# Performance work log

Measured on AMD Instinct MI355X. Metric: run time of the kernel, lower is better.

Reference implementation:

```python
import jax, jax.numpy as jnp
import numpy as np

NUM_HEADS = 8
WIN = 7  # local_window_size
HALF = WIN // 2


def setup_inputs() -> dict:
    key = jax.random.key(0)
    k1, k2, k3 = jax.random.split(key, 3)
    B, N, C = 1, 4096, 384  # N = T*H*W with T=4, H=W=32
    x = jax.random.normal(k1, (B, N, C), dtype=jnp.float32)
    w_qkv = jax.random.normal(k2, (C, 3 * C), dtype=jnp.float32) * 0.02
    w_proj = jax.random.normal(k3, (C, C), dtype=jnp.float32) * 0.02
    b_proj = jnp.zeros((C,), dtype=jnp.float32)
    return {"x": x, "w_qkv": w_qkv, "w_proj": w_proj, "b_proj": b_proj, "H": 32, "W": 32}


def _gather_windows(t):
    H, W = t.shape[3], t.shape[4]
    tp = jnp.pad(t, ((0, 0), (0, 0), (0, 0), (HALF, HALF), (HALF, HALF), (0, 0)))
    wins = [tp[:, :, :, dy:dy + H, dx:dx + W, :] for dy in range(WIN) for dx in range(WIN)]
    return jnp.stack(wins, axis=5)


def reference(x, w_qkv, w_proj, b_proj, H, W):
    B, N, C = x.shape
    nh, hd = NUM_HEADS, C // NUM_HEADS
    T = N // (H * W)
    scale = hd ** (-0.5)

    qkv = (x @ w_qkv).reshape(B, N, 3, nh, hd)
    # (B, nh, T, H, W, hd)
    q = qkv[:, :, 0].transpose(0, 2, 1, 3).reshape(B, nh, T, H, W, hd)
    k = qkv[:, :, 1].transpose(0, 2, 1, 3).reshape(B, nh, T, H, W, hd)
    v = qkv[:, :, 2].transpose(0, 2, 1, 3).reshape(B, nh, T, H, W, hd)

    kwin = _gather_windows(k)  # (B, nh, T, H, W, 49, hd); zeros at borders (NOT masked)
    vwin = _gather_windows(v)

    scores = jnp.einsum('bnthwd,bnthwkd->bnthwk', q, kwin) * scale
    attn = jax.nn.softmax(scores, axis=-1)  # zero-padded keys give score 0 -> weight exp(0)
    out = jnp.einsum('bnthwk,bnthwkd->bnthwd', attn, vwin)

    out = out.transpose(0, 2, 3, 4, 1, 5).reshape(B, N, C)
    return out @ w_proj + b_proj
```

## Files before the change

### kernel.cpp

```cpp
#include <hip/hip_runtime.h>
#include <hip/hip_bf16.h>
#include <math.h>

#define NH 8
#define HD 48
#define C_DIM 384
#define C3 1152
#define SCALE_F 0.14433756729740643f

typedef unsigned short ushort_t;
typedef __attribute__((ext_vector_type(8))) short short8;
typedef __attribute__((ext_vector_type(4))) float f32x4;

static __device__ __forceinline__ ushort_t bf16u(float f) {
    __hip_bfloat16 b = __float2bfloat16(f);
    return *(ushort_t*)&b;
}

__global__ __launch_bounds__(256) void split_bf16_kernel(const float* __restrict__ in,
                                                         ushort_t* __restrict__ hi,
                                                         ushort_t* __restrict__ lo,
                                                         int n4)
{
    const int i = blockIdx.x * 256 + threadIdx.x;
    if (i >= n4) return;
    const float4 v = ((const float4*)in)[i];
    const float f[4] = {v.x, v.y, v.z, v.w};
    ushort_t hb[4], lb[4];
    #pragma unroll
    for (int j = 0; j < 4; ++j) {
        __hip_bfloat16 h = __float2bfloat16(f[j]);
        __hip_bfloat16 l = __float2bfloat16(f[j] - __bfloat162float(h));
        hb[j] = *(ushort_t*)&h;
        lb[j] = *(ushort_t*)&l;
    }
    *(ushort4*)(hi + i * 4) = make_ushort4(hb[0], hb[1], hb[2], hb[3]);
    *(ushort4*)(lo + i * 4) = make_ushort4(lb[0], lb[1], lb[2], lb[3]);
}

__global__ __launch_bounds__(256) void split_wT_kernel(const float* __restrict__ w,
                                                       ushort_t* __restrict__ hiT,
                                                       ushort_t* __restrict__ loT,
                                                       int K, int N)
{
    const int idx = blockIdx.x * 256 + threadIdx.x;
    if (idx >= K * N) return;
    const int k = idx / N;
    const int n = idx - k * N;
    const float v = w[idx];
    __hip_bfloat16 h = __float2bfloat16(v);
    __hip_bfloat16 l = __float2bfloat16(v - __bfloat162float(h));
    hiT[n * K + k] = *(ushort_t*)&h;
    loT[n * K + k] = *(ushort_t*)&l;
}

__global__ __launch_bounds__(256) void gemm_mfma3(const ushort_t* __restrict__ Ah,
                                                  const ushort_t* __restrict__ Al,
                                                  const ushort_t* __restrict__ BhT,
                                                  const ushort_t* __restrict__ BlT,
                                                  const float* __restrict__ bias,
                                                  float* __restrict__ C,
                                                  int N, int K)
{
    __shared__ ushort_t sAh[128 * 40];
    __shared__ ushort_t sAl[128 * 40];
    __shared__ ushort_t sBh[64 * 40];
    __shared__ ushort_t sBl[64 * 40];

    const int tid = threadIdx.x;
    const int bm = blockIdx.x * 128;
    const int bn = blockIdx.y * 64;

    const int rowA = tid >> 2;
    const int slotA = (tid & 3) * 8;
    const int rowB = tid >> 2;
    const int slotB = (tid & 3) * 8;

    const ushort_t* gAh0 = Ah + (size_t)(bm + rowA) * K + slotA;
    const ushort_t* gAh1 = Ah + (size_t)(bm + rowA + 64) * K + slotA;
    const ushort_t* gAl0 = Al + (size_t)(bm + rowA) * K + slotA;
    const ushort_t* gAl1 = Al + (size_t)(bm + rowA + 64) * K + slotA;
    const ushort_t* gBh  = BhT + (size_t)(bn + rowB) * K + slotB;
    const ushort_t* gBl  = BlT + (size_t)(bn + rowB) * K + slotB;

    const int lane = tid & 63;
    const int wid = tid >> 6;
    const int wm = wid >> 1;
    const int wn = wid & 1;
    const int fr = lane & 15;
    const int kb = lane >> 4;
    const int aoff = (wm * 64 + fr) * 40 + kb * 8;
    const int boff = (wn * 32 + fr) * 40 + kb * 8;

    f32x4 acc[4][2] = {};

    for (int k0 = 0; k0 < K; k0 += 32) {
        const short8 va0 = *(const short8*)(gAh0 + k0);
        const short8 va1 = *(const short8*)(gAh1 + k0);
        const short8 vl0 = *(const short8*)(gAl0 + k0);
        const short8 vl1 = *(const short8*)(gAl1 + k0);
        const short8 vb0 = *(const short8*)(gBh + k0);
        const short8 vb1 = *(const short8*)(gBl + k0);
        *(short8*)&sAh[rowA * 40 + slotA]        = va0;
        *(short8*)&sAh[(rowA + 64) * 40 + slotA] = va1;
        *(short8*)&sAl[rowA * 40 + slotA]        = vl0;
        *(short8*)&sAl[(rowA + 64) * 40 + slotA] = vl1;
        *(short8*)&sBh[rowB * 40 + slotB]        = vb0;
        *(short8*)&sBl[rowB * 40 + slotB]        = vb1;
        __syncthreads();

        short8 ah[4], al[4], bh[2], bl[2];
        #pragma unroll
        for (int m = 0; m < 4; ++m) {
            ah[m] = *(const short8*)&sAh[aoff + m * 16 * 40];
            al[m] = *(const short8*)&sAl[aoff + m * 16 * 40];
        }
        #pragma unroll
        for (int n = 0; n < 2; ++n) {
            bh[n] = *(const short8*)&sBh[boff + n * 16 * 40];
            bl[n] = *(const short8*)&sBl[boff + n * 16 * 40];
        }
        #pragma unroll
        for (int m = 0; m < 4; ++m) {
            #pragma unroll
            for (int n = 0; n < 2; ++n) {
                acc[m][n] = __builtin_amdgcn_mfma_f32_16x16x32_bf16(ah[m], bh[n], acc[m][n], 0, 0, 0);
                acc[m][n] = __builtin_amdgcn_mfma_f32_16x16x32_bf16(ah[m], bl[n], acc[m][n], 0, 0, 0);
                acc[m][n] = __builtin_amdgcn_mfma_f32_16x16x32_bf16(al[m], bh[n], acc[m][n], 0, 0, 0);
            }
        }
        __syncthreads();
    }

    #pragma unroll
    for (int n = 0; n < 2; ++n) {
        const int col = bn + wn * 32 + n * 16 + fr;
        const float bv = bias ? bias[col] : 0.f;
        #pragma unroll
        for (int m = 0; m < 4; ++m) {
            const int r0 = bm + wm * 64 + m * 16 + kb * 4;
            #pragma unroll
            for (int r = 0; r < 4; ++r) {
                C[(size_t)(r0 + r) * N + col] = acc[m][n][r] + bv;
            }
        }
    }
}

__global__ __launch_bounds__(256) void gemm64(const float* __restrict__ A,
                                              const float* __restrict__ B,
                                              const float* __restrict__ bias,
                                              float* __restrict__ C,
                                              int M, int N, int K)
{
    __shared__ float As[64][17];
    __shared__ float Bs[16][64];

    const int tid = threadIdx.x;
    const int tx = tid & 15;
    const int ty = tid >> 4;
    const int bm = blockIdx.x * 64;
    const int bn = blockIdx.y * 64;
    const int arow = tid >> 2;
    const int acol = (tid & 3) << 2;
    const int brow = tid >> 4;
    const int bcol = (tid & 15) << 2;

    float acc[4][4] = {};

    for (int k0 = 0; k0 < K; k0 += 16) {
        const float4 a4 = *(const float4*)(A + (size_t)(bm + arow) * K + k0 + acol);
        const float4 b4 = *(const float4*)(B + (size_t)(k0 + brow) * N + bn + bcol);
        As[arow][acol + 0] = a4.x; As[arow][acol + 1] = a4.y;
        As[arow][acol + 2] = a4.z; As[arow][acol + 3] = a4.w;
        *(float4*)&Bs[brow][bcol] = b4;
        __syncthreads();
        #pragma unroll
        for (int kk = 0; kk < 16; ++kk) {
            const float a0 = As[ty * 4 + 0][kk];
            const float a1 = As[ty * 4 + 1][kk];
            const float a2 = As[ty * 4 + 2][kk];
            const float a3 = As[ty * 4 + 3][kk];
            const float4 b = *(const float4*)&Bs[kk][tx * 4];
            acc[0][0] = fmaf(a0, b.x, acc[0][0]); acc[0][1] = fmaf(a0, b.y, acc[0][1]);
            acc[0][2] = fmaf(a0, b.z, acc[0][2]); acc[0][3] = fmaf(a0, b.w, acc[0][3]);
            acc[1][0] = fmaf(a1, b.x, acc[1][0]); acc[1][1] = fmaf(a1, b.y, acc[1][1]);
            acc[1][2] = fmaf(a1, b.z, acc[1][2]); acc[1][3] = fmaf(a1, b.w, acc[1][3]);
            acc[2][0] = fmaf(a2, b.x, acc[2][0]); acc[2][1] = fmaf(a2, b.y, acc[2][1]);
            acc[2][2] = fmaf(a2, b.z, acc[2][2]); acc[2][3] = fmaf(a2, b.w, acc[2][3]);
            acc[3][0] = fmaf(a3, b.x, acc[3][0]); acc[3][1] = fmaf(a3, b.y, acc[3][1]);
            acc[3][2] = fmaf(a3, b.z, acc[3][2]); acc[3][3] = fmaf(a3, b.w, acc[3][3]);
        }
        __syncthreads();
    }

    float4 bb = {0.f, 0.f, 0.f, 0.f};
    if (bias) bb = *(const float4*)(bias + bn + tx * 4);
    #pragma unroll
    for (int i = 0; i < 4; ++i) {
        float4 o;
        o.x = acc[i][0] + bb.x; o.y = acc[i][1] + bb.y;
        o.z = acc[i][2] + bb.z; o.w = acc[i][3] + bb.w;
        *(float4*)(C + (size_t)(bm + ty * 4 + i) * N + bn + tx * 4) = o;
    }
}

#define KP_SHORTS 18432
#define PROW 72
__global__ __launch_bounds__(512) void local_attn_mfma5(const float* __restrict__ qkv,
                                                        ushort_t* __restrict__ outHi,
                                                        ushort_t* __restrict__ outLo)
{
    __shared__ ushort_t sKP[KP_SHORTS];
    __shared__ ushort_t sV[13504];
    __shared__ ushort_t sQ[2048];
    __shared__ float    sS[32 * 57];

    const int tid = threadIdx.x;
    const int b = blockIdx.x;
    const int t = b >> 8, h = (b >> 3) & 31, head = b & 7;

    if (tid < 288) {
        if (tid < 256) ((unsigned int*)(sKP + 17920))[tid] = 0u;
        else           ((unsigned int*)(sV + 13440))[tid - 256] = 0u;
    }

    #pragma unroll
    for (int it = 0; it < 2; ++it) {
        const int i = tid + it * 512;
        const int q = i >> 5, d = (i & 31) * 2;
        float2 v = make_float2(0.f, 0.f);
        if (d < 48)
            v = *(const float2*)(qkv + (size_t)((t << 10) + (h << 5) + q) * C3 + head * HD + d);
        const unsigned int pk = (unsigned int)bf16u(v.x * SCALE_F) | ((unsigned int)bf16u(v.y * SCALE_F) << 16);
        *(unsigned int*)&sQ[q * 64 + (d ^ ((q & 7) << 3))] = pk;
    }
    #pragma unroll
    for (int r = 0; r < 7; ++r) {
        const int hk = h + r - 3;
        const bool rowok = (unsigned)hk < 32u;
        const size_t rk = (size_t)((t << 10) + (hk << 5)) * C3 + C_DIM + head * HD;
        for (int i = tid; i < 1280; i += 512) {
            const int slot = i >> 5, d = (i & 31) * 2;
            const int c = slot - 3;
            float2 v = make_float2(0.f, 0.f);
            if (rowok && (unsigned)c < 32u && d < 48)
                v = *(const float2*)(qkv + rk + (size_t)c * C3 + d);
            const unsigned int pk = (unsigned int)bf16u(v.x) | ((unsigned int)bf16u(v.y) << 16);
            *(unsigned int*)&sKP[(r * 40 + slot) * 64 + (d ^ ((slot & 7) << 3))] = pk;
        }
    }
    __syncthreads();

    const int wv = tid >> 6, l = tid & 63, lr = l & 15, lc = l >> 4;

    float2 vreg[7][2];
    #pragma unroll
    for (int r = 0; r < 7; ++r) {
        const int hk = h + r - 3;
        const bool rowok = (unsigned)hk < 32u;
        const size_t rv = (size_t)((t << 10) + (hk << 5)) * C3 + 2 * C_DIM + head * HD;
        #pragma unroll
        for (int it = 0; it < 2; ++it) {
            const int i = tid + it * 512;
            float2 v = make_float2(0.f, 0.f);
            if (i < 960) {
                const int slot = i / 24;
                const int d = (i - slot * 24) * 2;
                const int c = slot - 3;
                if (rowok && (unsigned)c < 32u)
                    v = *(const float2*)(qkv + rv + (size_t)c * C3 + d);
            }
            vreg[r][it] = v;
        }
    }
    {
        short8 aq[2][2];
        #pragma unroll
        for (int fm = 0; fm < 2; ++fm) {
            const int q = fm * 16 + lr;
            aq[fm][0] = *(const short8*)&sQ[q * 64 + ((lc * 8) ^ ((q & 7) << 3))];
            aq[fm][1] = *(const short8*)&sQ[q * 64 + ((lc * 8 + 32) ^ ((q & 7) << 3))];
        }
        for (int u = wv; u < 21; u += 8) {
            const int r = u / 3, fn = u - r * 3;
            const int slot = fn * 16 + lr;
            const short8 b0 = *(const short8*)&sKP[(r * 40 + slot) * 64 + ((lc * 8) ^ ((slot & 7) << 3))];
            const short8 b1 = *(const short8*)&sKP[(r * 40 + slot) * 64 + ((lc * 8 + 32) ^ ((slot & 7) << 3))];
            f32x4 acc0 = {}, acc1 = {};
            acc0 = __builtin_amdgcn_mfma_f32_16x16x32_bf16(aq[0][0], b0, acc0, 0, 0, 0);
            acc0 = __builtin_amdgcn_mfma_f32_16x16x32_bf16(aq[0][1], b1, acc0, 0, 0, 0);
            acc1 = __builtin_amdgcn_mfma_f32_16x16x32_bf16(aq[1][0], b0, acc1, 0, 0, 0);
            acc1 = __builtin_amdgcn_mfma_f32_16x16x32_bf16(aq[1][1], b1, acc1, 0, 0, 0);
            #pragma unroll
            for (int reg = 0; reg < 4; ++reg) {
                const int q0 = lc * 4 + reg;
                const int dx0 = slot - q0;
                if (dx0 >= 0 && dx0 < 7) sS[q0 * 57 + r * 7 + dx0] = acc0[reg];
                const int q1 = 16 + lc * 4 + reg;
                const int dx1 = slot - q1;
                if (dx1 >= 0 && dx1 < 7) sS[q1 * 57 + r * 7 + dx1] = acc1[reg];
            }
        }
    }
    __syncthreads();

    #pragma unroll
    for (int r = 0; r < 7; ++r) {
        #pragma unroll
        for (int it = 0; it < 2; ++it) {
            const int i = tid + it * 512;
            if (i < 960) {
                const int slot = i / 24;
                const int d = (i - slot * 24) * 2;
                sV[(r * 48 + d) * 40 + slot]     = bf16u(vreg[r][it].x);
                sV[(r * 48 + d + 1) * 40 + slot] = bf16u(vreg[r][it].y);
            }
        }
    }
    if (tid < 32) {
        const int q = tid;
        float sv[49];
        #pragma unroll
        for (int j = 0; j < 49; ++j) sv[j] = sS[q * 57 + j];
        float mx = sv[0];
        #pragma unroll
        for (int j = 1; j < 49; ++j) mx = fmaxf(mx, sv[j]);
        float sum = 0.f;
        #pragma unroll
        for (int j = 0; j < 49; ++j) { sv[j] = __expf(sv[j] - mx); sum += sv[j]; }
        const float inv = 1.f / sum;
        #pragma unroll
        for (int j = 0; j < 49; ++j) {
            const int r = j / 7, dx = j - (j / 7) * 7;
            sKP[(r * 32 + q) * PROW + q + dx] = bf16u(sv[j] * inv);
        }
    } else {
        for (int i = tid - 32; i < 7 * 32 * PROW; i += 480) {
            const int row = i / PROW;
            const int col = i - row * PROW;
            const int q = row & 31;
            if ((unsigned)(col - q) >= 7u)
                sKP[i] = 0;
        }
    }
    __syncthreads();

    if (wv < 6) {
        const int fm = (wv >= 3) ? 1 : 0;
        const int fn = wv - fm * 3;
        const int q = fm * 16 + lr;
        const int dim = fn * 16 + lr;
        f32x4 acc = {};
        #pragma unroll
        for (int r = 0; r < 7; ++r) {
            const short8 a0 = *(const short8*)&sKP[(r * 32 + q) * PROW + lc * 8];
            const short8 a1 = *(const short8*)&sKP[(r * 32 + q) * PROW + lc * 8 + 32];
            const short8 b0 = *(const short8*)&sV[(r * 48 + dim) * 40 + lc * 8];
            const short8 b1 = *(const short8*)&sV[(r * 48 + dim) * 40 + lc * 8 + 32];
            acc = __builtin_amdgcn_mfma_f32_16x16x32_bf16(a0, b0, acc, 0, 0, 0);
            acc = __builtin_amdgcn_mfma_f32_16x16x32_bf16(a1, b1, acc, 0, 0, 0);
        }
        #pragma unroll
        for (int reg = 0; reg < 4; ++reg) {
            const int qq = fm * 16 + lc * 4 + reg;
            const int n = (t << 10) | (h << 5) | qq;
            const float o = acc[reg];
            __hip_bfloat16 hb = __float2bfloat16(o);
            __hip_bfloat16 lb = __float2bfloat16(o - __bfloat162float(hb));
            const size_t ob = (size_t)n * C_DIM + head * HD + dim;
            outHi[ob] = *(ushort_t*)&hb;
            outLo[ob] = *(ushort_t*)&lb;
        }
    }
}

__global__ __launch_bounds__(256) void local_attn16(const float* __restrict__ qkv,
                                                    float* __restrict__ out)
{
    const int tid = threadIdx.x;
    const int dlane = tid & 15;
    const int gid = blockIdx.x * 16 + (tid >> 4);
    const int head = gid & 7;
    const int n = gid >> 3;
    const int t = n >> 10;
    const int h = (n >> 5) & 31;
    const int w = n & 31;
    const float scale = SCALE_F;

    const float* qp = qkv + (size_t)n * C3 + head * HD;
    const float q0 = qp[dlane];
    const float q1 = qp[dlane + 16];
    const float q2 = qp[dlane + 32];

    const size_t base_k = (size_t)(C_DIM + head * HD);
    const size_t base_v = (size_t)(2 * C_DIM + head * HD);

    float s[49];
    #pragma unroll
    for (int p = 0; p < 49; ++p) {
        const int dy = p / 7, dx = p % 7;
        const int hk = h + dy - 3;
        const int wk = w + dx - 3;
        float sc = 0.f;
        if ((unsigned)hk < 32u && (unsigned)wk < 32u) {
            const int nk = (t << 10) | (hk << 5) | wk;
            const float* kp = qkv + (size_t)nk * C3 + base_k;
            float acc = q0 * kp[dlane];
            acc = fmaf(q1, kp[dlane + 16], acc);
            acc = fmaf(q2, kp[dlane + 32], acc);
            acc += __shfl_xor(acc, 1, 16);
            acc += __shfl_xor(acc, 2, 16);
            acc += __shfl_xor(acc, 4, 16);
            acc += __shfl_xor(acc, 8, 16);
            sc = acc * scale;
        }
        s[p] = sc;
    }

    float m = s[0];
    #pragma unroll
    for (int p = 1; p < 49; ++p) m = fmaxf(m, s[p]);
    float sum = 0.f;
    #pragma unroll
    for (int p = 0; p < 49; ++p) { s[p] = __expf(s[p] - m); sum += s[p]; }
    const float inv = 1.f / sum;

    float o0 = 0.f, o1 = 0.f, o2 = 0.f;
    #pragma unroll
    for (int p = 0; p < 49; ++p) {
        const int dy = p / 7, dx = p % 7;
        const int hk = h + dy - 3;
        const int wk = w + dx - 3;
        if ((unsigned)hk < 32u && (unsigned)wk < 32u) {
            const float wgt = s[p] * inv;
            const int nk = (t << 10) | (hk << 5) | wk;
            const float* vp = qkv + (size_t)nk * C3 + base_v;
            o0 = fmaf(wgt, vp[dlane],      o0);
            o1 = fmaf(wgt, vp[dlane + 16], o1);
            o2 = fmaf(wgt, vp[dlane + 32], o2);
        }
    }

    float* op = out + (size_t)n * C_DIM + head * HD;
    op[dlane]      = o0;
    op[dlane + 16] = o1;
    op[dlane + 32] = o2;
}

extern "C" void kernel_launch(void* const* d_in, const int* in_sizes, int n_in,
                              void* d_out, int out_size, void* d_ws, size_t ws_size,
                              hipStream_t stream)
{
    const float* x      = (const float*)d_in[0];
    const float* w_qkv  = (const float*)d_in[1];
    const float* w_proj = (const float*)d_in[2];
    const float* b_proj = (const float*)d_in[3];

    const int M = 4096;
    dim3 blk(256);

    const size_t NEED = 33226752;

    unsigned char* ws = (unsigned char*)d_ws;
    float* qkv = (float*)ws;
    float* att = (float*)(ws + 18874368);

    if (ws_size >= NEED) {
        ushort_t* Ah  = (ushort_t*)(ws + 25165824);
        ushort_t* Al  = (ushort_t*)(ws + 28311552);
        ushort_t* BhT = (ushort_t*)(ws + 31457280);
        ushort_t* BlT = (ushort_t*)(ws + 32342016);

        split_bf16_kernel<<<dim3(1536), blk, 0, stream>>>(x, Ah, Al, M * C_DIM / 4);
        split_wT_kernel<<<dim3((C_DIM * C3 + 255) / 256), blk, 0, stream>>>(w_qkv, BhT, BlT, C_DIM, C3);
        gemm_mfma3<<<dim3(M / 128, C3 / 64), blk, 0, stream>>>(Ah, Al, BhT, BlT, nullptr, qkv, C3, C_DIM);

        local_attn_mfma5<<<dim3(1024), dim3(512), 0, stream>>>(qkv, Ah, Al);

        split_wT_kernel<<<dim3((C_DIM * C_DIM + 255) / 256), blk, 0, stream>>>(w_proj, BhT, BlT, C_DIM, C_DIM);
        gemm_mfma3<<<dim3(M / 128, C_DIM / 64), blk, 0, stream>>>(Ah, Al, BhT, BlT, b_proj, (float*)d_out, C_DIM, C_DIM);
    } else {
        gemm64<<<dim3(M / 64, C3 / 64), blk, 0, stream>>>(x, w_qkv, nullptr, qkv, M, C3, C_DIM);
        local_attn16<<<dim3(2048), blk, 0, stream>>>(qkv, att);
        gemm64<<<dim3(M / 64, C_DIM / 64), blk, 0, stream>>>(att, w_proj, b_proj, (float*)d_out, M, C_DIM, C_DIM);
    }
}
```

Baseline: 91.83 us.

## Merge split kernels into one launch and remap GEMM blocks across XCDs

Combines the three fp32-to-bf16 hi/lo split kernels (x, w_qkv, w_proj) into a single launch, giving w_proj its own workspace buffers so it no longer has to be split after attention. Both GEMMs switch to a 1D grid with a workgroup remap that spreads consecutive block IDs across the 8 XCDs before decoding tile coordinates. The aim is fewer kernel launches and better L2 locality per XCD. It needs slightly more workspace, and the remap assumes the grid size is divisible by 8.

```diff
diff --git a/kernel.cpp b/kernel.cpp
--- a/kernel.cpp
+++ b/kernel.cpp
@@ -17,25 +17,50 @@
     return *(ushort_t*)&b;
 }
 
-__global__ __launch_bounds__(256) void split_bf16_kernel(const float* __restrict__ in,
-                                                         ushort_t* __restrict__ hi,
-                                                         ushort_t* __restrict__ lo,
-                                                         int n4)
-{
-    const int i = blockIdx.x * 256 + threadIdx.x;
-    if (i >= n4) return;
-    const float4 v = ((const float4*)in)[i];
-    const float f[4] = {v.x, v.y, v.z, v.w};
-    ushort_t hb[4], lb[4];
-    #pragma unroll
-    for (int j = 0; j < 4; ++j) {
-        __hip_bfloat16 h = __float2bfloat16(f[j]);
-        __hip_bfloat16 l = __float2bfloat16(f[j] - __bfloat162float(h));
-        hb[j] = *(ushort_t*)&h;
-        lb[j] = *(ushort_t*)&l;
-    }
-    *(ushort4*)(hi + i * 4) = make_ushort4(hb[0], hb[1], hb[2], hb[3]);
-    *(ushort4*)(lo + i * 4) = make_ushort4(lb[0], lb[1], lb[2], lb[3]);
+__global__ __launch_bounds__(256) void split_all(const float* __restrict__ x,
+                                                 ushort_t* __restrict__ hi,
+                                                 ushort_t* __restrict__ lo,
+                                                 const float* __restrict__ wq,
+                                                 ushort_t* __restrict__ qhiT,
+                                                 ushort_t* __restrict__ qloT,
+                                                 const float* __restrict__ wp,
+                                                 ushort_t* __restrict__ phiT,
+                                                 ushort_t* __restrict__ ploT)
+{
+    const int bidx = blockIdx.x;
+    if (bidx < 1536) {
+        const int i = bidx * 256 + threadIdx.x;
+        const float4 v = ((const float4*)x)[i];
+        const float f[4] = {v.x, v.y, v.z, v.w};
+        ushort_t hb[4], lb[4];
+        #pragma unroll
+        for (int j = 0; j < 4; ++j) {
+            __hip_bfloat16 h = __float2bfloat16(f[j]);
+            __hip_bfloat16 l = __float2bfloat16(f[j] - __bfloat162float(h));
+            hb[j] = *(ushort_t*)&h;
+            lb[j] = *(ushort_t*)&l;
+        }
+        *(ushort4*)(hi + i * 4) = make_ushort4(hb[0], hb[1], hb[2], hb[3]);
+        *(ushort4*)(lo + i * 4) = make_ushort4(lb[0], lb[1], lb[2], lb[3]);
+    } else if (bidx < 3264) {
+        const int idx = (bidx - 1536) * 256 + threadIdx.x;
+        const int k = idx / C3;
+        const int n = idx - k * C3;
+        const float v = wq[idx];
+        __hip_bfloat16 h = __float2bfloat16(v);
+        __hip_bfloat16 l = __float2bfloat16(v - __bfloat162float(h));
+        qhiT[n * C_DIM + k] = *(ushort_t*)&h;
+        qloT[n * C_DIM + k] = *(ushort_t*)&l;
+    } else {
+        const int idx = (bidx - 3264) * 256 + threadIdx.x;
+        const int k = idx / C_DIM;
+        const int n = idx - k * C_DIM;
+        const float v = wp[idx];
+        __hip_bfloat16 h = __float2bfloat16(v);
+        __hip_bfloat16 l = __float2bfloat16(v - __bfloat162float(h));
+        phiT[n * C_DIM + k] = *(ushort_t*)&h;
+        ploT[n * C_DIM + k] = *(ushort_t*)&l;
+    }
 }
 
 __global__ __launch_bounds__(256) void split_wT_kernel(const float* __restrict__ w,
@@ -60,7 +85,7 @@
                                                   const ushort_t* __restrict__ BlT,
                                                   const float* __restrict__ bias,
                                                   float* __restrict__ C,
-                                                  int N, int K)
+                                                  int N, int K, int gn)
 {
     __shared__ ushort_t sAh[128 * 40];
     __shared__ ushort_t sAl[128 * 40];
@@ -68,8 +93,13 @@
     __shared__ ushort_t sBl[64 * 40];
 
     const int tid = threadIdx.x;
-    const int bm = blockIdx.x * 128;
-    const int bn = blockIdx.y * 64;
+    const int nwg = gridDim.x;
+    const int orig = blockIdx.x;
+    const int wg = (orig & 7) * (nwg >> 3) + (orig >> 3);
+    const int bmi = wg / gn;
+    const int bni = wg - bmi * gn;
+    const int bm = bmi * 128;
+    const int bn = bni * 64;
 
     const int rowA = tid >> 2;
     const int slotA = (tid & 3) * 8;
@@ -460,7 +490,7 @@
     const int M = 4096;
     dim3 blk(256);
 
-    const size_t NEED = 33226752;
+    const size_t NEED = 33816576;
 
     unsigned char* ws = (unsigned char*)d_ws;
     float* qkv = (float*)ws;
@@ -471,15 +501,16 @@
         ushort_t* Al  = (ushort_t*)(ws + 28311552);
         ushort_t* BhT = (ushort_t*)(ws + 31457280);
         ushort_t* BlT = (ushort_t*)(ws + 32342016);
-
-        split_bf16_kernel<<<dim3(1536), blk, 0, stream>>>(x, Ah, Al, M * C_DIM / 4);
-        split_wT_kernel<<<dim3((C_DIM * C3 + 255) / 256), blk, 0, stream>>>(w_qkv, BhT, BlT, C_DIM, C3);
-        gemm_mfma3<<<dim3(M / 128, C3 / 64), blk, 0, stream>>>(Ah, Al, BhT, BlT, nullptr, qkv, C3, C_DIM);
+        ushort_t* PhT = (ushort_t*)(ws + 33226752);
+        ushort_t* PlT = (ushort_t*)(ws + 33521664);
+
+        split_all<<<dim3(3840), blk, 0, stream>>>(x, Ah, Al, w_qkv, BhT, BlT, w_proj, PhT, PlT);
+
+        gemm_mfma3<<<dim3(576), blk, 0, stream>>>(Ah, Al, BhT, BlT, nullptr, qkv, C3, C_DIM, 18);
 
         local_attn_mfma5<<<dim3(1024), dim3(512), 0, stream>>>(qkv, Ah, Al);
 
-        split_wT_kernel<<<dim3((C_DIM * C_DIM + 255) / 256), blk, 0, stream>>>(w_proj, BhT, BlT, C_DIM, C_DIM);
-        gemm_mfma3<<<dim3(M / 128, C_DIM / 64), blk, 0, stream>>>(Ah, Al, BhT, BlT, b_proj, (float*)d_out, C_DIM, C_DIM);
+        gemm_mfma3<<<dim3(192), blk, 0, stream>>>(Ah, Al, PhT, PlT, b_proj, (float*)d_out, C_DIM, C_DIM, 6);
     } else {
         gemm64<<<dim3(M / 64, C3 / 64), blk, 0, stream>>>(x, w_qkv, nullptr, qkv, M, C3, C_DIM);
         local_attn16<<<dim3(2048), blk, 0, stream>>>(qkv, att);
```

Result: faster. 85.41 us (median of 2 runs) (-7.0%).
